# Kernel optimization log

Hardware: AMD Instinct MI355X
Metric: run time of the kernel (lower is better)

Reference implementation:

```python
import jax, jax.numpy as jnp
import numpy as np

DIMS = [11, 20, 20, 30, 30, 40, 40, 40, 20, 10, 1]  # layer widths

def setup_inputs() -> dict:
    key = jax.random.key(0)
    ks = jax.random.split(key, 1 + 2 * (len(DIMS) - 1))
    inp = {"x": jax.random.normal(ks[0], (2000000, 11), dtype=jnp.float32)}
    for i in range(len(DIMS) - 1):
        d_in, d_out = DIMS[i], DIMS[i + 1]
        bound = 1.0 / np.sqrt(d_in)
        inp[f"W{i}"] = jax.random.uniform(ks[1 + 2 * i], (d_out, d_in), dtype=jnp.float32, minval=-bound, maxval=bound)
        inp[f"b{i}"] = jax.random.uniform(ks[2 + 2 * i], (d_out,), dtype=jnp.float32, minval=-bound, maxval=bound)
    return inp

def _swish(x):
    return x * jax.nn.sigmoid(x)

def reference(x, W0, b0, W1, b1, W2, b2, W3, b3, W4, b4, W5, b5, W6, b6, W7, b7, W8, b8, W9, b9):
    Ws = [W0, W1, W2, W3, W4, W5, W6, W7, W8, W9]
    bs = [b0, b1, b2, b3, b4, b5, b6, b7, b8, b9]
    h = x
    for i in range(9):  # 9 Linear+Swish blocks
        h = _swish(h @ Ws[i].T + bs[i])
    h = jax.nn.relu(h @ Ws[9].T + bs[9])  # final Linear(10,1) + ReLU
    return h.reshape(-1)
```

## Files before the change

kernel.cpp:

```cpp
#include <hip/hip_runtime.h>
#include <math.h>


typedef _Float16 half8 __attribute__((ext_vector_type(8)));
typedef _Float16 half4 __attribute__((ext_vector_type(4)));
typedef _Float16 half2 __attribute__((ext_vector_type(2)));
typedef float f32x4 __attribute__((ext_vector_type(4)));

#define ACT_W 72

__device__ __forceinline__ float swish_f(float a) {
    float e = __expf(-a);
    return a * __builtin_amdgcn_rcpf(1.0f + e);
}

__device__ __forceinline__ half8 make_frag(const float* __restrict__ W,
                                           const float* __restrict__ b,
                                           int IN, int OUT, int ot, int kt,
                                           int lr, int kg) {
    const int r = ot * 16 + lr;
    half8 h;
#pragma unroll
    for (int e = 0; e < 8; ++e) {
        const int k = kt * 32 + kg * 8 + e;
        float v = 0.0f;
        if (r < OUT) {
            if (k < IN)
                v = W[r * IN + k];
            else if (k == IN)
                v = b[r];
        }
        h[e] = (_Float16)v;
    }
    return h;
}

template <int NOT, int OUT>
__device__ __forceinline__ void epilogue(const f32x4 (&acc)[NOT],
                                         _Float16* wrp, int kg4) {
#pragma unroll
    for (int ot = 0; ot < NOT; ++ot) {
        float v[4];
#pragma unroll
        for (int r = 0; r < 4; ++r) {
            v[r] = swish_f(acc[ot][r]);
            if (ot == OUT / 16 && ot * 16 + kg4 + r == OUT) v[r] = 1.0f;
        }
        auto lo = __builtin_amdgcn_cvt_pkrtz(v[0], v[1]);
        auto hi = __builtin_amdgcn_cvt_pkrtz(v[2], v[3]);
        union {
            half4 h4;
            half2 h2[2];
        } u;
        u.h2[0] = __builtin_bit_cast(half2, lo);
        u.h2[1] = __builtin_bit_cast(half2, hi);
        *(half4*)(wrp + ot * 16) = u.h4;
    }
}

template <int NOT, int NKT, int OUT>
__device__ __forceinline__ void layer(const _Float16* __restrict__ wb,
                                      const _Float16* rdp, _Float16* wrp,
                                      int lane, int kg4) {
    f32x4 acc[NOT];
#pragma unroll
    for (int ot = 0; ot < NOT; ++ot) acc[ot] = (f32x4){0.f, 0.f, 0.f, 0.f};
#pragma unroll
    for (int kt = 0; kt < NKT; ++kt) {
        const half8 bf = *(const half8*)(rdp + kt * 32);
#pragma unroll
        for (int ot = 0; ot < NOT; ++ot) {
            const half8 wf =
                *(const half8*)(wb + (ot * NKT + kt) * 512 + lane * 8);
            acc[ot] = __builtin_amdgcn_mfma_f32_16x16x32_f16(wf, bf, acc[ot],
                                                             0, 0, 0);
        }
    }
    epilogue<NOT, OUT>(acc, wrp, kg4);
}

__global__ __launch_bounds__(256, 4) void longnet_mlp_r5(
    const float* __restrict__ x,
    const float* __restrict__ W0, const float* __restrict__ b0,
    const float* __restrict__ W1, const float* __restrict__ b1,
    const float* __restrict__ W2, const float* __restrict__ b2,
    const float* __restrict__ W3, const float* __restrict__ b3,
    const float* __restrict__ W4, const float* __restrict__ b4,
    const float* __restrict__ W5, const float* __restrict__ b5,
    const float* __restrict__ W6, const float* __restrict__ b6,
    const float* __restrict__ W7, const float* __restrict__ b7,
    const float* __restrict__ W8, const float* __restrict__ b8,
    const float* __restrict__ W9, const float* __restrict__ b9,
    float* __restrict__ out, int n) {
    __shared__ __align__(16) _Float16 s_w[29 * 512];
    __shared__ __align__(16) _Float16 s_act[4][16 * ACT_W];

    const int tid = threadIdx.x;
    const int lane = tid & 63;
    const int wave = tid >> 6;
    const int lr = lane & 15;
    const int kg = lane >> 4;
    const int kg4 = kg * 4;

    {
        const float* Wt[10] = {W0, W1, W2, W3, W4, W5, W6, W7, W8, W9};
        const float* bt[10] = {b0, b1, b2, b3, b4, b5, b6, b7, b8, b9};
        const int INs[10] = {11, 20, 20, 30, 30, 40, 40, 40, 20, 10};
        const int OUTs[10] = {20, 20, 30, 30, 40, 40, 40, 20, 10, 1};
        const int NOTs[10] = {2, 2, 2, 2, 3, 3, 3, 2, 1, 1};
        const int NKTs[10] = {1, 1, 1, 1, 1, 2, 2, 2, 1, 1};
        int f = 0;
        for (int L = 0; L < 10; ++L)
            for (int ot = 0; ot < NOTs[L]; ++ot)
                for (int kt = 0; kt < NKTs[L]; ++kt, ++f)
                    if ((f & 3) == wave) {
                        half8 h = make_frag(Wt[L], bt[L], INs[L], OUTs[L], ot,
                                            kt, lr, kg);
                        *(half8*)(s_w + f * 512 + lane * 8) = h;
                    }
    }

    _Float16* act = s_act[wave];
    {
        int* a32 = (int*)act;
#pragma unroll
        for (int i = 0; i < 9; ++i) a32[i * 64 + lane] = 0;
    }
    __syncthreads();

    const _Float16* rdp = act + lr * ACT_W + kg * 8;
    _Float16* wrp = act + lr * ACT_W + kg4;

    const int ntile = n >> 4;
    const int step = (int)gridDim.x * 4;

    for (int t = blockIdx.x * 4 + wave; t < ntile; t += step) {
        const int row0 = t * 16;

        half8 xb = {};
        if (kg < 2) {
            const float* xr = x + (size_t)(row0 + lr) * 11 + kg * 8;
#pragma unroll
            for (int e = 0; e < 8; ++e) {
                const int k = kg * 8 + e;
                float v = (k < 11) ? xr[e] : ((k == 11) ? 1.0f : 0.0f);
                xb[e] = (_Float16)v;
            }
        }

        {
            f32x4 acc[2];
#pragma unroll
            for (int ot = 0; ot < 2; ++ot) {
                const half8 wf = *(const half8*)(s_w + ot * 512 + lane * 8);
                acc[ot] = (f32x4){0.f, 0.f, 0.f, 0.f};
                acc[ot] = __builtin_amdgcn_mfma_f32_16x16x32_f16(wf, xb,
                                                                 acc[ot], 0,
                                                                 0, 0);
            }
            epilogue<2, 20>(acc, wrp, kg4);
        }
        layer<2, 1, 20>(s_w + 2 * 512, rdp, wrp, lane, kg4);
        layer<2, 1, 30>(s_w + 4 * 512, rdp, wrp, lane, kg4);
        layer<2, 1, 30>(s_w + 6 * 512, rdp, wrp, lane, kg4);
        layer<3, 1, 40>(s_w + 8 * 512, rdp, wrp, lane, kg4);
        layer<3, 2, 40>(s_w + 11 * 512, rdp, wrp, lane, kg4);
        layer<3, 2, 40>(s_w + 17 * 512, rdp, wrp, lane, kg4);
        layer<2, 2, 20>(s_w + 23 * 512, rdp, wrp, lane, kg4);
        layer<1, 1, 10>(s_w + 27 * 512, rdp, wrp, lane, kg4);

        {
            const half8 wf = *(const half8*)(s_w + 28 * 512 + lane * 8);
            const half8 bf = *(const half8*)rdp;
            f32x4 accF = (f32x4){0.f, 0.f, 0.f, 0.f};
            accF =
                __builtin_amdgcn_mfma_f32_16x16x32_f16(wf, bf, accF, 0, 0, 0);
            if (kg == 0) out[row0 + lr] = fmaxf(accF[0], 0.0f);
        }
    }
}

extern "C" void kernel_launch(void* const* d_in, const int* in_sizes, int n_in,
                              void* d_out, int out_size, void* d_ws, size_t ws_size,
                              hipStream_t stream) {
    const float* x = (const float*)d_in[0];
    const float* W0 = (const float*)d_in[1];
    const float* b0 = (const float*)d_in[2];
    const float* W1 = (const float*)d_in[3];
    const float* b1 = (const float*)d_in[4];
    const float* W2 = (const float*)d_in[5];
    const float* b2 = (const float*)d_in[6];
    const float* W3 = (const float*)d_in[7];
    const float* b3 = (const float*)d_in[8];
    const float* W4 = (const float*)d_in[9];
    const float* b4 = (const float*)d_in[10];
    const float* W5 = (const float*)d_in[11];
    const float* b5 = (const float*)d_in[12];
    const float* W6 = (const float*)d_in[13];
    const float* b6 = (const float*)d_in[14];
    const float* W7 = (const float*)d_in[15];
    const float* b7 = (const float*)d_in[16];
    const float* W8 = (const float*)d_in[17];
    const float* b8 = (const float*)d_in[18];
    const float* W9 = (const float*)d_in[19];
    const float* b9 = (const float*)d_in[20];
    float* out = (float*)d_out;

    const int n = in_sizes[0] / 11;
    const int grid = 1024;

    longnet_mlp_r5<<<grid, 256, 0, stream>>>(
        x, W0, b0, W1, b1, W2, b2, W3, b3, W4, b4, W5, b5, W6, b6, W7, b7, W8,
        b8, W9, b9, out, n);
}
```

Measured before the change: 200.1 us.

## Reorganize activation scratch into fragment-native layout and use 8-wave blocks

Per-wave activation storage moves from a padded row-major layout (stride 72) to a layout that matches the MFMA B-fragment order. Each lane now reads its operand as one contiguous half8 at lane*8, which avoids LDS bank conflicts and address arithmetic. Blocks grow to 512 threads with a grid of 768 and an occupancy hint of 6, so more waves share each block's copy of the staged weights. Accumulator zeroing is folded into the first MFMA through a zero constant. The costs are higher register pressure under the new launch bounds and a more intricate write-address formula in the epilogue.

```diff
diff --git a/kernel.cpp b/kernel.cpp
--- a/kernel.cpp
+++ b/kernel.cpp
@@ -6,8 +6,6 @@
 typedef _Float16 half4 __attribute__((ext_vector_type(4)));
 typedef _Float16 half2 __attribute__((ext_vector_type(2)));
 typedef float f32x4 __attribute__((ext_vector_type(4)));
-
-#define ACT_W 72
 
 __device__ __forceinline__ float swish_f(float a) {
     float e = __expf(-a);
@@ -37,14 +35,16 @@
 
 template <int NOT, int OUT>
 __device__ __forceinline__ void epilogue(const f32x4 (&acc)[NOT],
-                                         _Float16* wrp, int kg4) {
+                                         _Float16* act, int lr, int kg) {
+    const int kgl = kg & 1;
+    const int kgh = kg >> 1;
 #pragma unroll
     for (int ot = 0; ot < NOT; ++ot) {
         float v[4];
 #pragma unroll
         for (int r = 0; r < 4; ++r) {
             v[r] = swish_f(acc[ot][r]);
-            if (ot == OUT / 16 && ot * 16 + kg4 + r == OUT) v[r] = 1.0f;
+            if (ot == OUT / 16 && ot * 16 + kg * 4 + r == OUT) v[r] = 1.0f;
         }
         auto lo = __builtin_amdgcn_cvt_pkrtz(v[0], v[1]);
         auto hi = __builtin_amdgcn_cvt_pkrtz(v[2], v[3]);
@@ -54,32 +54,32 @@
         } u;
         u.h2[0] = __builtin_bit_cast(half2, lo);
         u.h2[1] = __builtin_bit_cast(half2, hi);
-        *(half4*)(wrp + ot * 16) = u.h4;
+        _Float16* p = act + (ot >> 1) * 512 +
+                      (((2 * ot + kgh) & 3) * 16 + lr) * 8 + kgl * 4;
+        *(half4*)p = u.h4;
     }
 }
 
 template <int NOT, int NKT, int OUT>
 __device__ __forceinline__ void layer(const _Float16* __restrict__ wb,
-                                      const _Float16* rdp, _Float16* wrp,
-                                      int lane, int kg4) {
+                                      _Float16* act, int lane, int lr, int kg,
+                                      f32x4 z4) {
     f32x4 acc[NOT];
 #pragma unroll
-    for (int ot = 0; ot < NOT; ++ot) acc[ot] = (f32x4){0.f, 0.f, 0.f, 0.f};
-#pragma unroll
     for (int kt = 0; kt < NKT; ++kt) {
-        const half8 bf = *(const half8*)(rdp + kt * 32);
+        const half8 bf = *(const half8*)(act + kt * 512 + lane * 8);
 #pragma unroll
         for (int ot = 0; ot < NOT; ++ot) {
             const half8 wf =
                 *(const half8*)(wb + (ot * NKT + kt) * 512 + lane * 8);
-            acc[ot] = __builtin_amdgcn_mfma_f32_16x16x32_f16(wf, bf, acc[ot],
-                                                             0, 0, 0);
-        }
-    }
-    epilogue<NOT, OUT>(acc, wrp, kg4);
-}
-
-__global__ __launch_bounds__(256, 4) void longnet_mlp_r5(
+            acc[ot] = __builtin_amdgcn_mfma_f32_16x16x32_f16(
+                wf, bf, kt == 0 ? z4 : acc[ot], 0, 0, 0);
+        }
+    }
+    epilogue<NOT, OUT>(acc, act, lr, kg);
+}
+
+__global__ __launch_bounds__(512, 6) void longnet_mlp_r6(
     const float* __restrict__ x,
     const float* __restrict__ W0, const float* __restrict__ b0,
     const float* __restrict__ W1, const float* __restrict__ b1,
@@ -93,14 +93,13 @@
     const float* __restrict__ W9, const float* __restrict__ b9,
     float* __restrict__ out, int n) {
     __shared__ __align__(16) _Float16 s_w[29 * 512];
-    __shared__ __align__(16) _Float16 s_act[4][16 * ACT_W];
+    __shared__ __align__(16) _Float16 s_act[8 * 1024];
 
     const int tid = threadIdx.x;
     const int lane = tid & 63;
     const int wave = tid >> 6;
     const int lr = lane & 15;
     const int kg = lane >> 4;
-    const int kg4 = kg * 4;
 
     {
         const float* Wt[10] = {W0, W1, W2, W3, W4, W5, W6, W7, W8, W9};
@@ -113,28 +112,26 @@
         for (int L = 0; L < 10; ++L)
             for (int ot = 0; ot < NOTs[L]; ++ot)
                 for (int kt = 0; kt < NKTs[L]; ++kt, ++f)
-                    if ((f & 3) == wave) {
+                    if ((f & 7) == wave) {
                         half8 h = make_frag(Wt[L], bt[L], INs[L], OUTs[L], ot,
                                             kt, lr, kg);
                         *(half8*)(s_w + f * 512 + lane * 8) = h;
                     }
     }
 
-    _Float16* act = s_act[wave];
+    _Float16* act = s_act + wave * 1024;
     {
         int* a32 = (int*)act;
 #pragma unroll
-        for (int i = 0; i < 9; ++i) a32[i * 64 + lane] = 0;
+        for (int i = 0; i < 8; ++i) a32[i * 64 + lane] = 0;
     }
     __syncthreads();
 
-    const _Float16* rdp = act + lr * ACT_W + kg * 8;
-    _Float16* wrp = act + lr * ACT_W + kg4;
-
+    const f32x4 z4 = (f32x4){0.f, 0.f, 0.f, 0.f};
     const int ntile = n >> 4;
-    const int step = (int)gridDim.x * 4;
-
-    for (int t = blockIdx.x * 4 + wave; t < ntile; t += step) {
+    const int step = (int)gridDim.x * 8;
+
+    for (int t = blockIdx.x * 8 + wave; t < ntile; t += step) {
         const int row0 = t * 16;
 
         half8 xb = {};
@@ -153,28 +150,25 @@
 #pragma unroll
             for (int ot = 0; ot < 2; ++ot) {
                 const half8 wf = *(const half8*)(s_w + ot * 512 + lane * 8);
-                acc[ot] = (f32x4){0.f, 0.f, 0.f, 0.f};
-                acc[ot] = __builtin_amdgcn_mfma_f32_16x16x32_f16(wf, xb,
-                                                                 acc[ot], 0,
-                                                                 0, 0);
+                acc[ot] = __builtin_amdgcn_mfma_f32_16x16x32_f16(wf, xb, z4,
+                                                                 0, 0, 0);
             }
-            epilogue<2, 20>(acc, wrp, kg4);
-        }
-        layer<2, 1, 20>(s_w + 2 * 512, rdp, wrp, lane, kg4);
-        layer<2, 1, 30>(s_w + 4 * 512, rdp, wrp, lane, kg4);
-        layer<2, 1, 30>(s_w + 6 * 512, rdp, wrp, lane, kg4);
-        layer<3, 1, 40>(s_w + 8 * 512, rdp, wrp, lane, kg4);
-        layer<3, 2, 40>(s_w + 11 * 512, rdp, wrp, lane, kg4);
-        layer<3, 2, 40>(s_w + 17 * 512, rdp, wrp, lane, kg4);
-        layer<2, 2, 20>(s_w + 23 * 512, rdp, wrp, lane, kg4);
-        layer<1, 1, 10>(s_w + 27 * 512, rdp, wrp, lane, kg4);
+            epilogue<2, 20>(acc, act, lr, kg);
+        }
+        layer<2, 1, 20>(s_w + 2 * 512, act, lane, lr, kg, z4);
+        layer<2, 1, 30>(s_w + 4 * 512, act, lane, lr, kg, z4);
+        layer<2, 1, 30>(s_w + 6 * 512, act, lane, lr, kg, z4);
+        layer<3, 1, 40>(s_w + 8 * 512, act, lane, lr, kg, z4);
+        layer<3, 2, 40>(s_w + 11 * 512, act, lane, lr, kg, z4);
+        layer<3, 2, 40>(s_w + 17 * 512, act, lane, lr, kg, z4);
+        layer<2, 2, 20>(s_w + 23 * 512, act, lane, lr, kg, z4);
+        layer<1, 1, 10>(s_w + 27 * 512, act, lane, lr, kg, z4);
 
         {
             const half8 wf = *(const half8*)(s_w + 28 * 512 + lane * 8);
-            const half8 bf = *(const half8*)rdp;
-            f32x4 accF = (f32x4){0.f, 0.f, 0.f, 0.f};
-            accF =
-                __builtin_amdgcn_mfma_f32_16x16x32_f16(wf, bf, accF, 0, 0, 0);
+            const half8 bf = *(const half8*)(act + lane * 8);
+            f32x4 accF =
+                __builtin_amdgcn_mfma_f32_16x16x32_f16(wf, bf, z4, 0, 0, 0);
             if (kg == 0) out[row0 + lr] = fmaxf(accF[0], 0.0f);
         }
     }
@@ -207,9 +201,9 @@
     float* out = (float*)d_out;
 
     const int n = in_sizes[0] / 11;
-    const int grid = 1024;
-
-    longnet_mlp_r5<<<grid, 256, 0, stream>>>(
+    const int grid = 768;
+
+    longnet_mlp_r6<<<grid, 512, 0, stream>>>(
         x, W0, b0, W1, b1, W2, b2, W3, b3, W4, b4, W5, b5, W6, b6, W7, b7, W8,
         b8, W9, b9, out, n);
 }
```

After: 316.7 us. 58.2% more time.
